# Optimization experiments

Measured on AMD Instinct MI355X. Metric: run time of the kernel, lower is better.

## Reference

```python
import jax, jax.numpy as jnp
import numpy as np

E = 2048  # embed_size == seq_len (required: edge_weight_fc maps last dim E -> 1 on the NxN scores)
B = 4
N = 2048


def setup_inputs() -> dict:
    key = jax.random.key(0)
    ks = jax.random.split(key, 12)
    s = 0.02
    inp = {
        "query": jax.random.normal(ks[0], (B, N, E), jnp.float32),
        "key": jax.random.normal(ks[1], (B, N, E), jnp.float32),
        "value": jax.random.normal(ks[2], (B, N, E), jnp.float32),
        "mask": jax.random.randint(ks[3], (B, N, N), 0, 2, jnp.int32),
        # nn.Linear weights stored torch-style as [out, in]
        "Wq": jax.random.normal(ks[4], (E, E), jnp.float32) * s,
        "bq": jnp.zeros((E,), jnp.float32),
        "Wk": jax.random.normal(ks[5], (E, E), jnp.float32) * s,
        "bk": jnp.zeros((E,), jnp.float32),
        "Wv": jax.random.normal(ks[6], (E, E), jnp.float32) * s,
        "bv": jnp.zeros((E,), jnp.float32),
        "We": jax.random.normal(ks[7], (1, E), jnp.float32) * s,  # edge_weight_fc: Linear(E, 1)
        "be": jnp.zeros((1,), jnp.float32),
        "Wo": jax.random.normal(ks[8], (E, E), jnp.float32) * s,
        "bo": jnp.zeros((E,), jnp.float32),
    }
    return inp


def reference(query, key, value, mask, Wq, bq, Wk, bk, Wv, bv, We, be, Wo, bo):
    # QKV projections (torch Linear: x @ W.T + b)
    Q = query @ Wq.T + bq                       # [B, N, E]
    K = key @ Wk.T + bk                         # [B, N, E]
    V = value @ Wv.T + bv                       # [B, N, E]
    scale = 1.0 / jnp.sqrt(jnp.asarray(E, jnp.float32))
    scores = jnp.einsum("bqe,bke->bqk", Q, K) * scale   # [B, N, N]
    scores = scores + mask.astype(scores.dtype) * (-1e9)
    # graph_structure is non-None -> learned sigmoid edge gate over score rows
    edge_w = jax.nn.sigmoid(scores @ We.T + be)          # [B, N, 1]
    scores = scores * edge_w
    attn = jax.nn.softmax(scores, axis=-1)               # [B, N, N]
    # dropout is identity in eval mode
    out = jnp.einsum("bqk,bke->bqe", attn, V)            # [B, N, E]
    return out @ Wo.T + bo
```

## Files before the change

### kernel.cpp

```cpp
#include <hip/hip_runtime.h>
#include <math.h>

#define BB 4
#define NN 2048
#define EE 2048

typedef __attribute__((ext_vector_type(8))) unsigned short ushort8;
typedef __attribute__((ext_vector_type(8))) __bf16 bf16x8;
typedef __attribute__((ext_vector_type(4))) float f32x4;

__device__ __forceinline__ unsigned short f2bf(float f) {
  unsigned int u = __float_as_uint(f);
  u = u + 0x7fffu + ((u >> 16) & 1u);
  return (unsigned short)(u >> 16);
}
__device__ __forceinline__ float bf2f(unsigned short h) {
  return __uint_as_float((unsigned)h << 16);
}

__device__ __forceinline__ void gload16(const void* g, void* l) {
  __builtin_amdgcn_global_load_lds(
      (__attribute__((address_space(1))) void*)g,
      (__attribute__((address_space(3))) void*)l, 16, 0, 0);
}

#define SCHED_FENCE() __builtin_amdgcn_sched_barrier(0)
#define BARRIER() do { SCHED_FENCE(); __builtin_amdgcn_s_barrier(); SCHED_FENCE(); } while (0)
#define WAIT_VM0() do { SCHED_FENCE(); asm volatile("s_waitcnt vmcnt(0)"); SCHED_FENCE(); } while (0)

__global__ __launch_bounds__(256) void k_f32_to_bf16(const float* __restrict__ in,
                                                     unsigned short* __restrict__ out) {
  size_t i = (size_t)blockIdx.x * 256 + threadIdx.x;
  const float4* ip = (const float4*)in;
  float4 a = ip[i * 2];
  float4 b = ip[i * 2 + 1];
  ushort8 o;
  o[0] = f2bf(a.x); o[1] = f2bf(a.y); o[2] = f2bf(a.z); o[3] = f2bf(a.w);
  o[4] = f2bf(b.x); o[5] = f2bf(b.y); o[6] = f2bf(b.z); o[7] = f2bf(b.w);
  *((ushort8*)out + i) = o;
}

__global__ __launch_bounds__(256) void k_transpose(const unsigned short* __restrict__ in,
                                                   unsigned short* __restrict__ out) {
  __shared__ __attribute__((aligned(16))) unsigned short tile[64][72];
  const long z = blockIdx.z;
  const long eb = (long)blockIdx.x * 64;
  const long nb = (long)blockIdx.y * 64;
  const unsigned short* ip = in + z * (long)NN * EE;
  unsigned short* op = out + z * (long)NN * EE;
  const int t = threadIdx.x;
  const int r = t >> 3;
  const int c = (t & 7) * 8;

  ushort8 u0 = *(const ushort8*)(ip + (nb + r) * EE + eb + c);
  ushort8 u1 = *(const ushort8*)(ip + (nb + 32 + r) * EE + eb + c);
  *(ushort8*)&tile[r][c] = u0;
  *(ushort8*)&tile[r + 32][c] = u1;
  __syncthreads();
  ushort8 o0, o1;
#pragma unroll
  for (int j = 0; j < 8; j++) { o0[j] = tile[c + j][r]; o1[j] = tile[c + j][r + 32]; }
  *(ushort8*)(op + (eb + r) * NN + nb + c) = o0;
  *(ushort8*)(op + (eb + r + 32) * NN + nb + c) = o1;
}

__global__ __launch_bounds__(256) void k_vecw(const float* __restrict__ Wq,
                                              const float* __restrict__ Wk,
                                              const float* __restrict__ bq,
                                              const float* __restrict__ bk,
                                              float* __restrict__ u,
                                              float* __restrict__ w2b,
                                              float* __restrict__ t4) {
  const int e = blockIdx.x * 256 + threadIdx.x;
  const int tt0 = blockIdx.y * 64;
  float su = 0.f, sw = 0.f;
#pragma unroll 4
  for (int i = 0; i < 64; i++) {
    int tt = tt0 + i;
    su += Wq[(long)tt * EE + e] * bk[tt];
    sw += Wk[(long)tt * EE + e] * bq[tt];
  }
  atomicAdd(&u[e], su);
  atomicAdd(&w2b[e], sw);
  if (blockIdx.x == 0 && threadIdx.x < 64) {
    int lane = threadIdx.x;
    float p = bq[tt0 + lane] * bk[tt0 + lane];
    for (int off = 32; off >= 1; off >>= 1) p += __shfl_down(p, off);
    if (lane == 0) atomicAdd(t4, p);
  }
}

__global__ __launch_bounds__(256) void k_cvec(const float* __restrict__ Wo,
                                              const float* __restrict__ bv,
                                              const float* __restrict__ bo,
                                              float* __restrict__ cv) {
  int row = blockIdx.x * 4 + (threadIdx.x >> 6);
  int lane = threadIdx.x & 63;
  float s = 0.f;
  for (int j = lane; j < EE; j += 64) s += Wo[(long)row * EE + j] * bv[j];
  for (int off = 32; off >= 1; off >>= 1) s += __shfl_down(s, off);
  if (lane == 0) cv[row] = s + bo[row];
}

__global__ __launch_bounds__(256) void k_rowterm(const unsigned short* __restrict__ qb,
                                                 const float* __restrict__ u,
                                                 const float* __restrict__ t4,
                                                 float* __restrict__ rt) {
  long row = (long)blockIdx.x * 4 + (threadIdx.x >> 6);
  int lane = threadIdx.x & 63;
  const unsigned short* qr = qb + row * EE;
  float s = 0.f;
#pragma unroll
  for (int it = 0; it < 4; ++it) {
    int e0 = it * 512 + lane * 8;
    ushort8 qv = *(const ushort8*)(qr + e0);
#pragma unroll
    for (int j = 0; j < 8; j++) s += bf2f(qv[j]) * u[e0 + j];
  }
  for (int off = 32; off >= 1; off >>= 1) s += __shfl_down(s, off);
  if (lane == 0) rt[row] = s + *t4;
}

template <int EPI>
__global__ __launch_bounds__(512, 4) void k_gemm128(
    const unsigned short* __restrict__ A, long lda, long sA,
    const unsigned short* __restrict__ Bm, long ldb, long sB,
    void* __restrict__ Cv, long ldc, long sC, int K,
    const float* __restrict__ bias,
    const int* __restrict__ mask, long sMask,
    const float* __restrict__ rt, float scale) {
  __shared__ __attribute__((aligned(16))) unsigned short As[2 * 8192];
  __shared__ __attribute__((aligned(16))) unsigned short Bs[2 * 8192];

  const int gx = gridDim.x, gy = gridDim.y;
  int lin = (int)blockIdx.x + gx * ((int)blockIdx.y + gy * (int)blockIdx.z);
  int nwg = gx * gy * (int)gridDim.z;
  int chunk = nwg >> 3;
  int sw = (lin & 7) * chunk + (lin >> 3);
  int bz = sw / (gx * gy); int rem = sw - bz * (gx * gy);
  int by = rem / gx; int bx = rem - by * gx;

  const long m0 = (long)by * 128;
  const long n0 = (long)bx * 128;
  const unsigned short* Ab = A + (long)bz * sA;
  const unsigned short* Bb = Bm + (long)bz * sB;

  const int t = threadIdx.x;
  const int lane = t & 63;
  const int w = t >> 6;
  const int wm = w >> 2;
  const int wn = w & 3;

  const int srow = t >> 3;
  const int scol = (((t & 7) * 16) ^ (((t >> 5) & 1) << 5)) >> 1;
  const unsigned short* Ga = Ab + (m0 + srow) * lda + scol;
  const unsigned short* Gb = Bb + (n0 + srow) * ldb + scol;
  const int ldst = t * 8;

#define STAGE(buf, tile) do { \
    const unsigned short* ga_ = Ga + (long)(tile) * 64; \
    const unsigned short* gb_ = Gb + (long)(tile) * 64; \
    unsigned short* la_ = As + (buf) * 8192 + ldst; \
    unsigned short* lb_ = Bs + (buf) * 8192 + ldst; \
    gload16(ga_, la_); gload16(ga_ + 64 * lda, la_ + 4096); \
    gload16(gb_, lb_); gload16(gb_ + 64 * ldb, lb_ + 4096); \
  } while (0)

  const int r = lane & 15;
  const int q = lane >> 4;
  const int rb2 = ((r * 128 + q * 16) ^ ((r & 4) << 3)) >> 1;
  const int aBase = wm * 4096 + rb2;
  const int bBase = wn * 2048 + rb2;

  f32x4 acc[4][2] = {};
  bf16x8 a[4][2], b[2][2];
  const int J = K >> 6;

  STAGE(0, 0);
  WAIT_VM0();
  BARRIER();

  for (int j = 0; j < J; ++j) {
    const int c = j & 1;
    const unsigned short* Ac = As + c * 8192;
    const unsigned short* Bc = Bs + c * 8192;
#pragma unroll
    for (int mi = 0; mi < 4; mi++)
#pragma unroll
      for (int kk = 0; kk < 2; kk++)
        a[mi][kk] = *(const bf16x8*)(Ac + aBase + mi * 1024 + kk * 32);
#pragma unroll
    for (int ni = 0; ni < 2; ni++)
#pragma unroll
      for (int kk = 0; kk < 2; kk++)
        b[ni][kk] = *(const bf16x8*)(Bc + bBase + ni * 1024 + kk * 32);
    if (j + 1 < J) STAGE(c ^ 1, j + 1);
    __builtin_amdgcn_s_setprio(1);
#pragma unroll
    for (int mi = 0; mi < 4; mi++)
#pragma unroll
      for (int ni = 0; ni < 2; ni++)
#pragma unroll
        for (int kk = 0; kk < 2; kk++)
          acc[mi][ni] = __builtin_amdgcn_mfma_f32_16x16x32_bf16(
              a[mi][kk], b[ni][kk], acc[mi][ni], 0, 0, 0);
    __builtin_amdgcn_s_setprio(0);
    WAIT_VM0();
    BARRIER();
  }
#undef STAGE

  const int cr0 = wm * 64 + (q << 2);
  const int cc0 = wn * 32 + r;
  if (EPI == 0) {
    unsigned short* Co = (unsigned short*)Cv + (long)bz * sC;
#pragma unroll
    for (int mi = 0; mi < 4; mi++)
#pragma unroll
      for (int rr = 0; rr < 4; rr++) {
        long row = m0 + cr0 + mi * 16 + rr;
#pragma unroll
        for (int ni = 0; ni < 2; ni++) {
          long col = n0 + cc0 + ni * 16;
          float v = acc[mi][ni][rr];
          if (bias) v += bias[col];
          Co[row * ldc + col] = f2bf(v);
        }
      }
  } else if (EPI == 1) {
    float* Co = (float*)Cv + (long)bz * sC;
    const int* Mp = mask + (long)bz * sMask;
    const float* rtb = rt + (long)bz * NN;
#pragma unroll
    for (int mi = 0; mi < 4; mi++)
#pragma unroll
      for (int rr = 0; rr < 4; rr++) {
        long row = m0 + cr0 + mi * 16 + rr;
        float rv = rtb[row];
#pragma unroll
        for (int ni = 0; ni < 2; ni++) {
          long col = n0 + cc0 + ni * 16;
          Co[row * ldc + col] = (acc[mi][ni][rr] + rv) * scale + (float)Mp[row * ldc + col] * -1e9f;
        }
      }
  } else {
    float* Co = (float*)Cv + (long)bz * sC;
#pragma unroll
    for (int mi = 0; mi < 4; mi++)
#pragma unroll
      for (int rr = 0; rr < 4; rr++) {
        long row = m0 + cr0 + mi * 16 + rr;
#pragma unroll
        for (int ni = 0; ni < 2; ni++) {
          long col = n0 + cc0 + ni * 16;
          Co[row * ldc + col] = acc[mi][ni][rr] + bias[col];
        }
      }
  }
}

__global__ __launch_bounds__(256) void k_edge_softmax(float* __restrict__ scores,
                                                      const float* __restrict__ We,
                                                      const float* __restrict__ be) {
  __shared__ float r1[4], r2[4], r3[4];
  const long row = blockIdx.x;
  float* srow = scores + row * (long)NN;
  const int t = threadIdx.x;
  const int lane = t & 63;
  const int w = t >> 6;

  float4 a = *(const float4*)(srow + t * 8);
  float4 b = *(const float4*)(srow + t * 8 + 4);
  float s[8] = {a.x, a.y, a.z, a.w, b.x, b.y, b.z, b.w};
  float4 wa = *(const float4*)(We + t * 8);
  float4 wb = *(const float4*)(We + t * 8 + 4);
  float wv[8] = {wa.x, wa.y, wa.z, wa.w, wb.x, wb.y, wb.z, wb.w};

  float dot = 0.f;
#pragma unroll
  for (int j = 0; j < 8; j++) dot += s[j] * wv[j];
#pragma unroll
  for (int off = 32; off >= 1; off >>= 1) dot += __shfl_down(dot, off);
  if (lane == 0) r1[w] = dot;
  __syncthreads();
  float edot = r1[0] + r1[1] + r1[2] + r1[3] + be[0];
  float edge = 1.0f / (1.0f + expf(-edot));

  float mx = -3.4e38f;
#pragma unroll
  for (int j = 0; j < 8; j++) { s[j] *= edge; mx = fmaxf(mx, s[j]); }
#pragma unroll
  for (int off = 32; off >= 1; off >>= 1) mx = fmaxf(mx, __shfl_down(mx, off));
  if (lane == 0) r2[w] = mx;
  __syncthreads();
  mx = fmaxf(fmaxf(r2[0], r2[1]), fmaxf(r2[2], r2[3]));

  float sum = 0.f;
  float p[8];
#pragma unroll
  for (int j = 0; j < 8; j++) { p[j] = expf(s[j] - mx); sum += p[j]; }
#pragma unroll
  for (int off = 32; off >= 1; off >>= 1) sum += __shfl_down(sum, off);
  if (lane == 0) r3[w] = sum;
  __syncthreads();
  sum = r3[0] + r3[1] + r3[2] + r3[3];
  float inv = 1.0f / sum;

  ushort8 o;
#pragma unroll
  for (int j = 0; j < 8; j++) o[j] = f2bf(p[j] * inv);
  *(ushort8*)((unsigned short*)srow + t * 8) = o;
}

extern "C" void kernel_launch(void* const* d_in, const int* in_sizes, int n_in,
                              void* d_out, int out_size, void* d_ws, size_t ws_size,
                              hipStream_t stream) {
  (void)in_sizes; (void)n_in; (void)out_size; (void)ws_size;
  const float* query = (const float*)d_in[0];
  const float* key_  = (const float*)d_in[1];
  const float* value = (const float*)d_in[2];
  const int*   mask  = (const int*)d_in[3];
  const float* Wq = (const float*)d_in[4];
  const float* bq = (const float*)d_in[5];
  const float* Wk = (const float*)d_in[6];
  const float* bk = (const float*)d_in[7];
  const float* Wv = (const float*)d_in[8];
  const float* bv = (const float*)d_in[9];
  const float* We = (const float*)d_in[10];
  const float* be = (const float*)d_in[11];
  const float* Wo = (const float*)d_in[12];
  const float* bo = (const float*)d_in[13];
  float* out = (float*)d_out;

  const long WSZ = (long)EE * EE;
  char* ws = (char*)d_ws;
  unsigned short* WkT = (unsigned short*)(ws);
  unsigned short* Wob = WkT + WSZ;
  unsigned short* WqT = (unsigned short*)(ws + 16777216L);
  unsigned short* WvT = WqT + WSZ;
  unsigned short* W2T = (unsigned short*)(ws + 33554432L);
  unsigned short* W3T = W2T + WSZ;
  unsigned short* Wqb = (unsigned short*)(ws + 50331648L);
  unsigned short* Wkb = Wqb + WSZ;
  unsigned short* Wvb = Wqb + 2 * WSZ;
  unsigned short* qb  = (unsigned short*)(ws + 79691776L);
  unsigned short* kb  = (unsigned short*)(ws + 114294784L);
  unsigned short* vb  = (unsigned short*)(ws + 148897792L);
  unsigned short* Tb  = vb;
  unsigned short* Vt2 = (unsigned short*)(ws + 183500800L);
  unsigned short* Vt2T = qb;
  float* SC   = (float*)(ws);
  float* cvec = (float*)(ws + 219938816L);
  float* uvec = cvec + EE;
  float* w2b  = cvec + 2 * EE;
  float* t4   = cvec + 3 * EE;
  float* rt   = cvec + 3 * EE + 64;

  const float scale = 1.0f / sqrtf((float)EE);
  dim3 blk(256), blk5(512);

  k_f32_to_bf16<<<2048, blk, 0, stream>>>(Wq, Wqb);
  k_f32_to_bf16<<<2048, blk, 0, stream>>>(Wk, Wkb);
  k_f32_to_bf16<<<2048, blk, 0, stream>>>(Wv, Wvb);
  k_f32_to_bf16<<<2048, blk, 0, stream>>>(Wo, Wob);
  k_transpose<<<dim3(32, 32, 1), blk, 0, stream>>>(Wkb, WkT);
  k_transpose<<<dim3(32, 32, 1), blk, 0, stream>>>(Wqb, WqT);
  k_transpose<<<dim3(32, 32, 1), blk, 0, stream>>>(Wvb, WvT);
  hipMemsetAsync(uvec, 0, (2 * EE + 64) * sizeof(float), stream);
  k_vecw<<<dim3(8, 32), blk, 0, stream>>>(Wq, Wk, bq, bk, uvec, w2b, t4);
  k_cvec<<<512, blk, 0, stream>>>(Wo, bv, bo, cvec);
  k_gemm128<0><<<dim3(16, 16, 2), blk5, 0, stream>>>(WkT, EE, WSZ, WqT, EE, WSZ,
      W2T, EE, WSZ, EE, nullptr, nullptr, 0, nullptr, 0.f);
  k_f32_to_bf16<<<8192, blk, 0, stream>>>(query, qb);
  k_f32_to_bf16<<<8192, blk, 0, stream>>>(key_, kb);
  k_f32_to_bf16<<<8192, blk, 0, stream>>>(value, vb);
  k_gemm128<0><<<dim3(16, 64, 1), blk5, 0, stream>>>(vb, EE, 0, W3T, EE, 0,
      Vt2, EE, 0, EE, nullptr, nullptr, 0, nullptr, 0.f);
  k_gemm128<0><<<dim3(16, 64, 1), blk5, 0, stream>>>(qb, EE, 0, W2T, EE, 0,
      Tb, EE, 0, EE, w2b, nullptr, 0, nullptr, 0.f);
  k_rowterm<<<2048, blk, 0, stream>>>(qb, uvec, t4, rt);
  k_transpose<<<dim3(32, 32, BB), blk, 0, stream>>>(Vt2, Vt2T);
  k_gemm128<1><<<dim3(16, 16, BB), blk5, 0, stream>>>(Tb, EE, (long)NN * EE, kb, EE, (long)NN * EE,
      SC, NN, (long)NN * NN, EE, nullptr, mask, (long)NN * NN, rt, scale);
  k_edge_softmax<<<BB * NN, blk, 0, stream>>>(SC, We, be);
  k_gemm128<2><<<dim3(16, 16, BB), blk5, 0, stream>>>((const unsigned short*)SC, 2 * NN,
      (long)NN * 2 * NN, Vt2T, NN, (long)EE * NN, out, EE, (long)NN * EE, NN,
      cvec, nullptr, 0, nullptr, 0.f);
}
```

Baseline: 504.9 us.

## Add 256x256 pipelined GEMM, fuse edge dot into scores epilogue, bf16 scores

Adds a 256x256-tile GEMM with a finer-grained interleaved prefetch schedule and uses it for the activation GEMMs, replacing the 128x128 kernel there. The scores GEMM epilogue now writes bf16 scores and accumulates the edge-gate dot product per row through LDS and global atomics. That removes the fp32 score round trip and the dot-product pass in softmax. Weight conversion and transpose are fused into a single kernel. The bf16 scores before the sigmoid gating and softmax may reduce accuracy, and the atomic accumulation is not deterministic.

Result: faster. 482.0 us (-4.5%).

```diff
diff --git a/kernel.cpp b/kernel.cpp
--- a/kernel.cpp
+++ b/kernel.cpp
@@ -26,7 +26,7 @@
 
 #define SCHED_FENCE() __builtin_amdgcn_sched_barrier(0)
 #define BARRIER() do { SCHED_FENCE(); __builtin_amdgcn_s_barrier(); SCHED_FENCE(); } while (0)
-#define WAIT_VM0() do { SCHED_FENCE(); asm volatile("s_waitcnt vmcnt(0)"); SCHED_FENCE(); } while (0)
+#define WAIT_VM(N) do { SCHED_FENCE(); asm volatile("s_waitcnt vmcnt(" #N ")"); SCHED_FENCE(); } while (0)
 
 __global__ __launch_bounds__(256) void k_f32_to_bf16(const float* __restrict__ in,
                                                      unsigned short* __restrict__ out) {
@@ -38,6 +38,33 @@
   o[0] = f2bf(a.x); o[1] = f2bf(a.y); o[2] = f2bf(a.z); o[3] = f2bf(a.w);
   o[4] = f2bf(b.x); o[5] = f2bf(b.y); o[6] = f2bf(b.z); o[7] = f2bf(b.w);
   *((ushort8*)out + i) = o;
+}
+
+__global__ __launch_bounds__(256) void k_trf2b(const float* __restrict__ in,
+                                               unsigned short* __restrict__ out) {
+  __shared__ __attribute__((aligned(16))) unsigned short tile[64][72];
+  const long eb = (long)blockIdx.x * 64;
+  const long nb = (long)blockIdx.y * 64;
+  const int t = threadIdx.x;
+  const int r = t >> 3;
+  const int c = (t & 7) * 8;
+
+  const float* p0 = in + (nb + r) * (long)EE + eb + c;
+  const float* p1 = in + (nb + 32 + r) * (long)EE + eb + c;
+  float4 a0 = *(const float4*)p0, a1 = *(const float4*)(p0 + 4);
+  float4 b0 = *(const float4*)p1, b1 = *(const float4*)(p1 + 4);
+  unsigned short* t0 = &tile[r][c];
+  unsigned short* t1 = &tile[r + 32][c];
+  t0[0] = f2bf(a0.x); t0[1] = f2bf(a0.y); t0[2] = f2bf(a0.z); t0[3] = f2bf(a0.w);
+  t0[4] = f2bf(a1.x); t0[5] = f2bf(a1.y); t0[6] = f2bf(a1.z); t0[7] = f2bf(a1.w);
+  t1[0] = f2bf(b0.x); t1[1] = f2bf(b0.y); t1[2] = f2bf(b0.z); t1[3] = f2bf(b0.w);
+  t1[4] = f2bf(b1.x); t1[5] = f2bf(b1.y); t1[6] = f2bf(b1.z); t1[7] = f2bf(b1.w);
+  __syncthreads();
+  ushort8 o0, o1;
+#pragma unroll
+  for (int j = 0; j < 8; j++) { o0[j] = tile[c + j][r]; o1[j] = tile[c + j][r + 32]; }
+  *(ushort8*)(out + (eb + r) * (long)NN + nb + c) = o0;
+  *(ushort8*)(out + (eb + r + 32) * (long)NN + nb + c) = o1;
 }
 
 __global__ __launch_bounds__(256) void k_transpose(const unsigned short* __restrict__ in,
@@ -121,17 +148,12 @@
   if (lane == 0) rt[row] = s + *t4;
 }
 
-template <int EPI>
 __global__ __launch_bounds__(512, 4) void k_gemm128(
     const unsigned short* __restrict__ A, long lda, long sA,
     const unsigned short* __restrict__ Bm, long ldb, long sB,
-    void* __restrict__ Cv, long ldc, long sC, int K,
-    const float* __restrict__ bias,
-    const int* __restrict__ mask, long sMask,
-    const float* __restrict__ rt, float scale) {
+    unsigned short* __restrict__ Co, long ldc, long sC, int K) {
   __shared__ __attribute__((aligned(16))) unsigned short As[2 * 8192];
   __shared__ __attribute__((aligned(16))) unsigned short Bs[2 * 8192];
-
   const int gx = gridDim.x, gy = gridDim.y;
   int lin = (int)blockIdx.x + gx * ((int)blockIdx.y + gy * (int)blockIdx.z);
   int nwg = gx * gy * (int)gridDim.z;
@@ -144,12 +166,10 @@
   const long n0 = (long)bx * 128;
   const unsigned short* Ab = A + (long)bz * sA;
   const unsigned short* Bb = Bm + (long)bz * sB;
-
   const int t = threadIdx.x;
   const int lane = t & 63;
   const int w = t >> 6;
-  const int wm = w >> 2;
-  const int wn = w & 3;
+  const int wm = w >> 2, wn = w & 3;
 
   const int srow = t >> 3;
   const int scol = (((t & 7) * 16) ^ (((t >> 5) & 1) << 5)) >> 1;
@@ -175,11 +195,9 @@
   f32x4 acc[4][2] = {};
   bf16x8 a[4][2], b[2][2];
   const int J = K >> 6;
-
   STAGE(0, 0);
-  WAIT_VM0();
+  WAIT_VM(0);
   BARRIER();
-
   for (int j = 0; j < J; ++j) {
     const int c = j & 1;
     const unsigned short* Ac = As + c * 8192;
@@ -205,22 +223,166 @@
           acc[mi][ni] = __builtin_amdgcn_mfma_f32_16x16x32_bf16(
               a[mi][kk], b[ni][kk], acc[mi][ni], 0, 0, 0);
     __builtin_amdgcn_s_setprio(0);
-    WAIT_VM0();
+    WAIT_VM(0);
     BARRIER();
   }
 #undef STAGE
-
   const int cr0 = wm * 64 + (q << 2);
   const int cc0 = wn * 32 + r;
+#pragma unroll
+  for (int mi = 0; mi < 4; mi++)
+#pragma unroll
+    for (int rr = 0; rr < 4; rr++) {
+      long row = m0 + cr0 + mi * 16 + rr;
+#pragma unroll
+      for (int ni = 0; ni < 2; ni++)
+        Co[(long)bz * sC + row * ldc + n0 + cc0 + ni * 16] = f2bf(acc[mi][ni][rr]);
+    }
+}
+
+template <int EPI>
+__global__ __launch_bounds__(512, 2) void k_gemm256(
+    const unsigned short* __restrict__ A, long lda, long sA,
+    const unsigned short* __restrict__ Bm, long ldb, long sB,
+    void* __restrict__ Cv, long ldc, long sC, int K,
+    const float* __restrict__ bias,
+    const int* __restrict__ mask, long sMask,
+    const float* __restrict__ rt, float scale,
+    const float* __restrict__ We, float* __restrict__ edot) {
+  __shared__ __attribute__((aligned(16))) unsigned short As[2 * 16384];
+  __shared__ __attribute__((aligned(16))) unsigned short Bs[2 * 16384];
+
+  const int gx = gridDim.x, gy = gridDim.y;
+  int lin = (int)blockIdx.x + gx * ((int)blockIdx.y + gy * (int)blockIdx.z);
+  int nwg = gx * gy * (int)gridDim.z;
+  int chunk = nwg >> 3;
+  int sw = (lin & 7) * chunk + (lin >> 3);
+  int bz = sw / (gx * gy); int rem = sw - bz * (gx * gy);
+  int by = rem / gx; int bx = rem - by * gx;
+
+  const long m0 = (long)by * 256;
+  const long n0 = (long)bx * 256;
+  const unsigned short* Ab = A + (long)bz * sA;
+  const unsigned short* Bb = Bm + (long)bz * sB;
+
+  const int t = threadIdx.x;
+  const int lane = t & 63;
+  const int w = t >> 6;
+  const int wm = w >> 2;
+  const int wn = w & 3;
+
+  const int p0 = t * 16;
+  const int q0 = p0 ^ (((p0 >> 9) & 1) << 5);
+  const int srow = ((q0 >> 10) >> 1) * 16 + ((q0 >> 6) & 15);
+  const int scol = ((q0 >> 10) & 1) * 32 + ((q0 & 63) >> 1);
+  const unsigned short* Ga = Ab + (m0 + srow) * lda + scol;
+  const unsigned short* Gb = Bb + (n0 + srow) * ldb + scol;
+  const int ldst = t * 8;
+
+#define STAGE_A(buf, h, tile) do { \
+    const unsigned short* g_ = Ga + (long)(tile) * 64 + (long)(h) * 128 * lda; \
+    unsigned short* l_ = As + (buf) * 16384 + (h) * 8192 + ldst; \
+    gload16(g_, l_); gload16(g_ + 64 * lda, l_ + 4096); \
+  } while (0)
+#define STAGE_B(buf, h, tile) do { \
+    const unsigned short* g_ = Gb + (long)(tile) * 64 + (long)(h) * 128 * ldb; \
+    unsigned short* l_ = Bs + (buf) * 16384 + (h) * 8192 + ldst; \
+    gload16(g_, l_); gload16(g_ + 64 * ldb, l_ + 4096); \
+  } while (0)
+
+  const int r = lane & 15;
+  const int q = lane >> 4;
+  const int c2h = ((q * 16) ^ (((lane >> 3) & 1) << 5)) >> 1;
+  const int aBase = wm * 8192 + r * 32 + c2h;
+  const int bBase = (wn >> 1) * 8192 + (wn & 1) * 4096 + r * 32 + c2h;
+
+#define RD_A(bp, mbase) do { \
+    _Pragma("unroll") for (int mi = 0; mi < 4; mi++) \
+    _Pragma("unroll") for (int kk = 0; kk < 2; kk++) \
+      a[mi][kk] = *(const bf16x8*)((bp) + aBase + ((mbase) + mi) * 1024 + kk * 512); \
+  } while (0)
+#define RD_B(bp, nbase) do { \
+    _Pragma("unroll") for (int ni = 0; ni < 2; ni++) \
+    _Pragma("unroll") for (int kk = 0; kk < 2; kk++) \
+      b[(nbase) + ni][kk] = *(const bf16x8*)((bp) + bBase + ((nbase) + ni) * 1024 + kk * 512); \
+  } while (0)
+#define MFMA_Q(mbase, nbase) do { \
+    BARRIER(); \
+    __builtin_amdgcn_s_setprio(1); \
+    _Pragma("unroll") for (int mi = 0; mi < 4; mi++) \
+    _Pragma("unroll") for (int ni = 0; ni < 2; ni++) \
+    _Pragma("unroll") for (int kk = 0; kk < 2; kk++) \
+      acc[(mbase) + mi][(nbase) + ni] = __builtin_amdgcn_mfma_f32_16x16x32_bf16( \
+          a[mi][kk], b[(nbase) + ni][kk], acc[(mbase) + mi][(nbase) + ni], 0, 0, 0); \
+    __builtin_amdgcn_s_setprio(0); \
+    BARRIER(); \
+  } while (0)
+
+  f32x4 acc[8][4] = {};
+  bf16x8 a[4][2], b[4][2];
+  const unsigned short* A0 = As;
+  const unsigned short* B0 = Bs;
+  const unsigned short* A1 = As + 16384;
+  const unsigned short* B1 = Bs + 16384;
+  const int J = K >> 7;
+
+  STAGE_B(0, 0, 0); STAGE_B(0, 1, 0);
+  STAGE_A(0, 0, 0); STAGE_A(0, 1, 0);
+  STAGE_B(1, 0, 1); STAGE_B(1, 1, 1);
+  WAIT_VM(4);
+  BARRIER();
+
+  for (int j = 0; j < J; ++j) {
+    const int t0 = 2 * j, t1 = 2 * j + 1;
+    const bool pf = (j + 1 < J);
+
+    RD_A(A0, 0); RD_B(B0, 0);
+    STAGE_A(1, 0, t1);
+    MFMA_Q(0, 0);
+
+    RD_B(B0, 2);
+    STAGE_A(1, 1, t1);
+    MFMA_Q(0, 2);
+
+    RD_A(A0, 4);
+    if (pf) STAGE_B(0, 0, t0 + 2);
+    MFMA_Q(4, 0);
+
+    if (pf) { STAGE_B(0, 1, t0 + 2); WAIT_VM(4); } else { WAIT_VM(0); }
+    MFMA_Q(4, 2);
+
+    RD_A(A1, 0); RD_B(B1, 0);
+    if (pf) STAGE_A(0, 0, t0 + 2);
+    MFMA_Q(0, 0);
+
+    RD_B(B1, 2);
+    if (pf) STAGE_A(0, 1, t0 + 2);
+    MFMA_Q(0, 2);
+
+    RD_A(A1, 4);
+    if (pf) STAGE_B(1, 0, t1 + 2);
+    MFMA_Q(4, 0);
+
+    if (pf) { STAGE_B(1, 1, t1 + 2); WAIT_VM(4); }
+    MFMA_Q(4, 2);
+  }
+#undef STAGE_A
+#undef STAGE_B
+#undef RD_A
+#undef RD_B
+#undef MFMA_Q
+
+  const int cr0 = wm * 128 + (q << 2);
+  const int cc0 = wn * 64 + r;
   if (EPI == 0) {
     unsigned short* Co = (unsigned short*)Cv + (long)bz * sC;
 #pragma unroll
-    for (int mi = 0; mi < 4; mi++)
+    for (int mi = 0; mi < 8; mi++)
 #pragma unroll
       for (int rr = 0; rr < 4; rr++) {
         long row = m0 + cr0 + mi * 16 + rr;
 #pragma unroll
-        for (int ni = 0; ni < 2; ni++) {
+        for (int ni = 0; ni < 4; ni++) {
           long col = n0 + cc0 + ni * 16;
           float v = acc[mi][ni][rr];
           if (bias) v += bias[col];
@@ -228,30 +390,53 @@
         }
       }
   } else if (EPI == 1) {
-    float* Co = (float*)Cv + (long)bz * sC;
+    unsigned short* Co = (unsigned short*)Cv + (long)bz * sC;
     const int* Mp = mask + (long)bz * sMask;
     const float* rtb = rt + (long)bz * NN;
-#pragma unroll
-    for (int mi = 0; mi < 4; mi++)
+    float* edpart = (float*)As;
+    if (t < 256) edpart[t] = 0.f;
+    __syncthreads();
+    float wec[4];
+#pragma unroll
+    for (int ni = 0; ni < 4; ni++) wec[ni] = We[n0 + cc0 + ni * 16];
+#pragma unroll
+    for (int mi = 0; mi < 8; mi++) {
+      float pr[4];
 #pragma unroll
       for (int rr = 0; rr < 4; rr++) {
         long row = m0 + cr0 + mi * 16 + rr;
         float rv = rtb[row];
-#pragma unroll
-        for (int ni = 0; ni < 2; ni++) {
+        float pv = 0.f;
+#pragma unroll
+        for (int ni = 0; ni < 4; ni++) {
           long col = n0 + cc0 + ni * 16;
-          Co[row * ldc + col] = (acc[mi][ni][rr] + rv) * scale + (float)Mp[row * ldc + col] * -1e9f;
+          float sm = (acc[mi][ni][rr] + rv) * scale + (float)Mp[row * ldc + col] * -1e9f;
+          Co[row * ldc + col] = f2bf(sm);
+          pv += sm * wec[ni];
         }
+        pr[rr] = pv;
       }
+#pragma unroll
+      for (int mask_ = 1; mask_ < 16; mask_ <<= 1)
+#pragma unroll
+        for (int rr = 0; rr < 4; rr++) pr[rr] += __shfl_xor(pr[rr], mask_);
+      if (r == 0) {
+#pragma unroll
+        for (int rr = 0; rr < 4; rr++)
+          atomicAdd(&edpart[cr0 + mi * 16 + rr], pr[rr]);
+      }
+    }
+    __syncthreads();
+    if (t < 256) atomicAdd(&edot[(long)bz * NN + m0 + t], edpart[t]);
   } else {
     float* Co = (float*)Cv + (long)bz * sC;
 #pragma unroll
-    for (int mi = 0; mi < 4; mi++)
+    for (int mi = 0; mi < 8; mi++)
 #pragma unroll
       for (int rr = 0; rr < 4; rr++) {
         long row = m0 + cr0 + mi * 16 + rr;
 #pragma unroll
-        for (int ni = 0; ni < 2; ni++) {
+        for (int ni = 0; ni < 4; ni++) {
           long col = n0 + cc0 + ni * 16;
           Co[row * ldc + col] = acc[mi][ni][rr] + bias[col];
         }
@@ -259,36 +444,22 @@
   }
 }
 
-__global__ __launch_bounds__(256) void k_edge_softmax(float* __restrict__ scores,
-                                                      const float* __restrict__ We,
+__global__ __launch_bounds__(256) void k_edge_softmax(unsigned short* __restrict__ attn,
+                                                      const float* __restrict__ edot,
                                                       const float* __restrict__ be) {
-  __shared__ float r1[4], r2[4], r3[4];
+  __shared__ float r2[4], r3[4];
   const long row = blockIdx.x;
-  float* srow = scores + row * (long)NN;
+  unsigned short* srow = attn + row * (long)NN;
   const int t = threadIdx.x;
   const int lane = t & 63;
   const int w = t >> 6;
 
-  float4 a = *(const float4*)(srow + t * 8);
-  float4 b = *(const float4*)(srow + t * 8 + 4);
-  float s[8] = {a.x, a.y, a.z, a.w, b.x, b.y, b.z, b.w};
-  float4 wa = *(const float4*)(We + t * 8);
-  float4 wb = *(const float4*)(We + t * 8 + 4);
-  float wv[8] = {wa.x, wa.y, wa.z, wa.w, wb.x, wb.y, wb.z, wb.w};
-
-  float dot = 0.f;
-#pragma unroll
-  for (int j = 0; j < 8; j++) dot += s[j] * wv[j];
-#pragma unroll
-  for (int off = 32; off >= 1; off >>= 1) dot += __shfl_down(dot, off);
-  if (lane == 0) r1[w] = dot;
-  __syncthreads();
-  float edot = r1[0] + r1[1] + r1[2] + r1[3] + be[0];
-  float edge = 1.0f / (1.0f + expf(-edot));
-
+  float edge = 1.0f / (1.0f + expf(-(edot[row] + be[0])));
+  ushort8 v = *(const ushort8*)(srow + t * 8);
+  float s[8];
   float mx = -3.4e38f;
 #pragma unroll
-  for (int j = 0; j < 8; j++) { s[j] *= edge; mx = fmaxf(mx, s[j]); }
+  for (int j = 0; j < 8; j++) { s[j] = bf2f(v[j]) * edge; mx = fmaxf(mx, s[j]); }
 #pragma unroll
   for (int off = 32; off >= 1; off >>= 1) mx = fmaxf(mx, __shfl_down(mx, off));
   if (lane == 0) r2[w] = mx;
@@ -309,7 +480,7 @@
   ushort8 o;
 #pragma unroll
   for (int j = 0; j < 8; j++) o[j] = f2bf(p[j] * inv);
-  *(ushort8*)((unsigned short*)srow + t * 8) = o;
+  *(ushort8*)(srow + t * 8) = o;
 }
 
 extern "C" void kernel_launch(void* const* d_in, const int* in_sizes, int n_in,
@@ -336,54 +507,50 @@
   char* ws = (char*)d_ws;
   unsigned short* WkT = (unsigned short*)(ws);
   unsigned short* Wob = WkT + WSZ;
-  unsigned short* WqT = (unsigned short*)(ws + 16777216L);
-  unsigned short* WvT = WqT + WSZ;
+  unsigned short* WqT = WkT + 2 * WSZ;
+  unsigned short* WvT = WkT + 3 * WSZ;
   unsigned short* W2T = (unsigned short*)(ws + 33554432L);
   unsigned short* W3T = W2T + WSZ;
-  unsigned short* Wqb = (unsigned short*)(ws + 50331648L);
-  unsigned short* Wkb = Wqb + WSZ;
-  unsigned short* Wvb = Wqb + 2 * WSZ;
+  unsigned short* attn = (unsigned short*)(ws);
   unsigned short* qb  = (unsigned short*)(ws + 79691776L);
   unsigned short* kb  = (unsigned short*)(ws + 114294784L);
   unsigned short* vb  = (unsigned short*)(ws + 148897792L);
   unsigned short* Tb  = vb;
   unsigned short* Vt2 = (unsigned short*)(ws + 183500800L);
   unsigned short* Vt2T = qb;
-  float* SC   = (float*)(ws);
   float* cvec = (float*)(ws + 219938816L);
   float* uvec = cvec + EE;
   float* w2b  = cvec + 2 * EE;
   float* t4   = cvec + 3 * EE;
   float* rt   = cvec + 3 * EE + 64;
+  float* edot = rt + (long)BB * NN;
 
   const float scale = 1.0f / sqrtf((float)EE);
   dim3 blk(256), blk5(512);
 
-  k_f32_to_bf16<<<2048, blk, 0, stream>>>(Wq, Wqb);
-  k_f32_to_bf16<<<2048, blk, 0, stream>>>(Wk, Wkb);
-  k_f32_to_bf16<<<2048, blk, 0, stream>>>(Wv, Wvb);
+  k_trf2b<<<dim3(32, 32), blk, 0, stream>>>(Wk, WkT);
+  k_trf2b<<<dim3(32, 32), blk, 0, stream>>>(Wq, WqT);
+  k_trf2b<<<dim3(32, 32), blk, 0, stream>>>(Wv, WvT);
   k_f32_to_bf16<<<2048, blk, 0, stream>>>(Wo, Wob);
-  k_transpose<<<dim3(32, 32, 1), blk, 0, stream>>>(Wkb, WkT);
-  k_transpose<<<dim3(32, 32, 1), blk, 0, stream>>>(Wqb, WqT);
-  k_transpose<<<dim3(32, 32, 1), blk, 0, stream>>>(Wvb, WvT);
   hipMemsetAsync(uvec, 0, (2 * EE + 64) * sizeof(float), stream);
+  hipMemsetAsync(edot, 0, (long)BB * NN * sizeof(float), stream);
   k_vecw<<<dim3(8, 32), blk, 0, stream>>>(Wq, Wk, bq, bk, uvec, w2b, t4);
   k_cvec<<<512, blk, 0, stream>>>(Wo, bv, bo, cvec);
-  k_gemm128<0><<<dim3(16, 16, 2), blk5, 0, stream>>>(WkT, EE, WSZ, WqT, EE, WSZ,
-      W2T, EE, WSZ, EE, nullptr, nullptr, 0, nullptr, 0.f);
+  k_gemm128<<<dim3(16, 16, 2), blk5, 0, stream>>>(WkT, EE, WSZ, WqT, EE, WSZ,
+      W2T, EE, WSZ, EE);
   k_f32_to_bf16<<<8192, blk, 0, stream>>>(query, qb);
   k_f32_to_bf16<<<8192, blk, 0, stream>>>(key_, kb);
   k_f32_to_bf16<<<8192, blk, 0, stream>>>(value, vb);
-  k_gemm128<0><<<dim3(16, 64, 1), blk5, 0, stream>>>(vb, EE, 0, W3T, EE, 0,
-      Vt2, EE, 0, EE, nullptr, nullptr, 0, nullptr, 0.f);
-  k_gemm128<0><<<dim3(16, 64, 1), blk5, 0, stream>>>(qb, EE, 0, W2T, EE, 0,
-      Tb, EE, 0, EE, w2b, nullptr, 0, nullptr, 0.f);
+  k_gemm256<0><<<dim3(8, 32, 1), blk5, 0, stream>>>(vb, EE, 0, W3T, EE, 0,
+      Vt2, EE, 0, EE, nullptr, nullptr, 0, nullptr, 0.f, nullptr, nullptr);
+  k_gemm256<0><<<dim3(8, 32, 1), blk5, 0, stream>>>(qb, EE, 0, W2T, EE, 0,
+      Tb, EE, 0, EE, w2b, nullptr, 0, nullptr, 0.f, nullptr, nullptr);
   k_rowterm<<<2048, blk, 0, stream>>>(qb, uvec, t4, rt);
   k_transpose<<<dim3(32, 32, BB), blk, 0, stream>>>(Vt2, Vt2T);
-  k_gemm128<1><<<dim3(16, 16, BB), blk5, 0, stream>>>(Tb, EE, (long)NN * EE, kb, EE, (long)NN * EE,
-      SC, NN, (long)NN * NN, EE, nullptr, mask, (long)NN * NN, rt, scale);
-  k_edge_softmax<<<BB * NN, blk, 0, stream>>>(SC, We, be);
-  k_gemm128<2><<<dim3(16, 16, BB), blk5, 0, stream>>>((const unsigned short*)SC, 2 * NN,
-      (long)NN * 2 * NN, Vt2T, NN, (long)EE * NN, out, EE, (long)NN * EE, NN,
-      cvec, nullptr, 0, nullptr, 0.f);
-}
+  k_gemm256<1><<<dim3(8, 8, BB), blk5, 0, stream>>>(Tb, EE, (long)NN * EE, kb, EE, (long)NN * EE,
+      attn, NN, (long)NN * NN, EE, nullptr, mask, (long)NN * NN, rt, scale, We, edot);
+  k_edge_softmax<<<BB * NN, blk, 0, stream>>>(attn, edot, be);
+  k_gemm256<2><<<dim3(8, 8, BB), blk5, 0, stream>>>(attn, NN, (long)NN * NN,
+      Vt2T, NN, (long)EE * NN, out, EE, (long)NN * EE, NN,
+      cvec, nullptr, 0, nullptr, 0.f, nullptr, nullptr);
+}
```
